# Kernel optimization log

Hardware: AMD Instinct MI355X
Metric: run time of the kernel (lower is better)

The kernel has to match this reference:

```python
import jax, jax.numpy as jnp
import numpy as np
import math

D_MODEL = 1024
NHEAD = 16
FACTOR = 5


def setup_inputs() -> dict:
    key = jax.random.key(0)
    kq, kk, kv = jax.random.split(key, 3)
    B, L = 4, 2048
    Q = jax.random.normal(kq, (B, L, D_MODEL), dtype=jnp.float32)
    K = jax.random.normal(kk, (B, L, D_MODEL), dtype=jnp.float32)
    V = jax.random.normal(kv, (B, L, D_MODEL), dtype=jnp.float32)
    return {"Q": Q, "K": K, "V": V}


def reference(Q, K, V):
    B, q_len, _ = Q.shape
    k_len = K.shape[1]
    head_dim = D_MODEL // NHEAD
    scale = 1.0 / math.sqrt(head_dim)

    # [B, H, L, Dh]
    Qh = Q.reshape(B, q_len, NHEAD, head_dim).transpose(0, 2, 1, 3)
    Kh = K.reshape(B, k_len, NHEAD, head_dim).transpose(0, 2, 1, 3)
    Vh = V.reshape(B, k_len, NHEAD, head_dim).transpose(0, 2, 1, 3)

    # Dense scores for KL-based query selection
    scores = jnp.einsum('bhqd,bhkd->bhqk', Qh, Kh) * scale
    logp = jax.nn.log_softmax(scores, axis=-1)
    probs = jnp.exp(logp)
    # KL(p || uniform) = sum p * (log p + log k_len)
    kl_div = jnp.sum(probs * (logp + jnp.log(jnp.float32(k_len))), axis=-1)  # [B,H,Q]

    top_u = min(int(FACTOR * math.log(q_len)), q_len)
    _, indices = jax.lax.top_k(kl_div, top_u)  # [B,H,U]

    # Gather selected queries
    Q_sparse = jnp.take_along_axis(Qh, indices[..., None], axis=2)  # [B,H,U,Dh]
    scores_sparse = jnp.einsum('bhud,bhkd->bhuk', Q_sparse, Kh) * scale
    attn_weights = jax.nn.softmax(scores_sparse, axis=-1)  # dropout p=0 (eval)
    output_sparse = jnp.einsum('bhuk,bhkd->bhud', attn_weights, Vh)

    # Scatter back into full-length output (non-selected queries are zero)
    b_idx = jnp.arange(B)[:, None, None]
    h_idx = jnp.arange(NHEAD)[None, :, None]
    output_full = jnp.zeros_like(Qh).at[b_idx, h_idx, indices].set(output_sparse)

    output = output_full.transpose(0, 2, 1, 3).reshape(B, q_len, D_MODEL)
    return output, attn_weights
```

## Files before the change

### kernel.cpp

```cpp
#include <hip/hip_runtime.h>
#include <math.h>

#define LQ 2048
#define DM 1024
#define NH 16
#define DH 64
#define UU 38
#define NBH 64
#define SCALE 0.125f

typedef _Float16 f16x8 __attribute__((ext_vector_type(8)));
typedef float f32x4 __attribute__((ext_vector_type(4)));
typedef float f32x2 __attribute__((ext_vector_type(2)));

#if __has_builtin(__builtin_amdgcn_exp2f)
#define EXP2F(x) __builtin_amdgcn_exp2f(x)
#else
#define EXP2F(x) exp2f(x)
#endif

#define GL2LDS16(gp, lp)                                           \
  __builtin_amdgcn_global_load_lds(                                \
      (const __attribute__((address_space(1))) void*)(gp),         \
      (__attribute__((address_space(3))) void*)(lp), 16, 0, 0)

#define F_OFF_SEL   4194304
#define F_OFF_L3    4204032
#define F_OFF_MASK  4213760
#define F_OFF_LPART 4344832
#define F_OFF_KSP   7146496
#define F_NEED      40700928ull

__global__ __launch_bounds__(256) void ksplit_kernel(const float* __restrict__ K,
                                                     _Float16* __restrict__ ksp,
                                                     float* __restrict__ outz) {
  int idx = blockIdx.x * 256 + threadIdx.x;
  int p = idx & 7;
  int k = (idx >> 3) & 63;
  int kc = (idx >> 9) & 31;
  int bh = idx >> 14;
  int b = bh >> 4, h = bh & 15;
  const float* src = K + ((size_t)(b * LQ + kc * 64 + k)) * DM + h * DH + (p ^ (k & 7)) * 8;
  float4 x0 = *(const float4*)src;
  float4 x1 = *(const float4*)(src + 4);
  f16x8 hi, lo;
#define KCV(i, xx) { float x_ = (xx); _Float16 hh = (_Float16)x_; hi[i] = hh; lo[i] = (_Float16)(x_ - (float)hh); }
  KCV(0, x0.x) KCV(1, x0.y) KCV(2, x0.z) KCV(3, x0.w)
  KCV(4, x1.x) KCV(5, x1.y) KCV(6, x1.z) KCV(7, x1.w)
#undef KCV
  _Float16* base = ksp + ((size_t)(bh * 32 + kc)) * 8192;
  *(f16x8*)(base + k * 64 + p * 8) = hi;
  *(f16x8*)(base + 4096 + k * 64 + p * 8) = lo;

  float4 z = {0.f, 0.f, 0.f, 0.f};
  *(float4*)(outz + (size_t)idx * 8) = z;
  *(float4*)(outz + (size_t)idx * 8 + 4) = z;
}

__global__ __launch_bounds__(256) void kl_mfma2(const float* __restrict__ Q,
                                                const _Float16* __restrict__ ksp,
                                                double* __restrict__ lt) {
  int bh = blockIdx.x & 63;
  int qc = (blockIdx.x >> 6) & 15;
  int sp = blockIdx.x >> 10;
  int b = bh >> 4, h = bh & 15;
  int t = threadIdx.x;
  int lane = t & 63, w = t >> 6;
  int quad = lane >> 4, l15 = lane & 15;

  __shared__ __align__(16) _Float16 kbuf[8192];

  f16x8 ahi[2][2], alo[2][2];
  {
    const float* qrow = Q + ((size_t)(b * LQ + qc * 128)) * DM + h * DH;
#pragma unroll
    for (int qt = 0; qt < 2; ++qt)
#pragma unroll
      for (int c = 0; c < 2; ++c) {
        const float* p = qrow + (size_t)(w * 32 + qt * 16 + l15) * DM + c * 32 + quad * 8;
        float4 x0 = *(const float4*)p;
        float4 x1 = *(const float4*)(p + 4);
        f16x8 hi, lo;
#define QCV(i, xx) { float x_ = (xx); _Float16 hh = (_Float16)x_; hi[i] = hh; lo[i] = (_Float16)(x_ - (float)hh); }
        QCV(0, x0.x) QCV(1, x0.y) QCV(2, x0.z) QCV(3, x0.w)
        QCV(4, x1.x) QCV(5, x1.y) QCV(6, x1.z) QCV(7, x1.w)
#undef QCV
        ahi[qt][c] = hi;
        alo[qt][c] = lo;
      }
  }

  int bsw0 = quad ^ (l15 & 7);
  int bsw1 = (quad + 4) ^ (l15 & 7);
  const float C1 = 0.18033688011112042f;

  double l64[2][4], t64[2][4];
#pragma unroll
  for (int qt = 0; qt < 2; ++qt)
#pragma unroll
    for (int r = 0; r < 4; ++r) { l64[qt][r] = 0.0; t64[qt][r] = 0.0; }

  const _Float16* khiA = kbuf;
  const _Float16* kloA = kbuf + 2048;
  const _Float16* khiB = kbuf + 4096;
  const _Float16* kloB = kbuf + 6144;

  const char* gp = (const char*)(ksp + ((size_t)(bh * 32 + sp * 16)) * 8192) + t * 16;
  char* ldsA = (char*)kbuf + w * 1024;
  char* ldsB = (char*)kbuf + 8192 + w * 1024;

#define KLSTEP(KHI, KLO)                                                        \
  _Pragma("unroll")                                                             \
  for (int kt = 0; kt < 2; ++kt) {                                              \
    int key = kt * 16 + l15;                                                    \
    f16x8 bhi0 = *(const f16x8*)((KHI) + key * 64 + bsw0 * 8);                  \
    f16x8 bhi1 = *(const f16x8*)((KHI) + key * 64 + bsw1 * 8);                  \
    f16x8 blo0 = *(const f16x8*)((KLO) + key * 64 + bsw0 * 8);                  \
    f16x8 blo1 = *(const f16x8*)((KLO) + key * 64 + bsw1 * 8);                  \
    _Pragma("unroll")                                                           \
    for (int qt = 0; qt < 2; ++qt) {                                            \
      f32x4 cacc = {0.f, 0.f, 0.f, 0.f};                                        \
      __builtin_amdgcn_s_setprio(1);                                            \
      cacc = __builtin_amdgcn_mfma_f32_16x16x32_f16(alo[qt][0], bhi0, cacc, 0, 0, 0); \
      cacc = __builtin_amdgcn_mfma_f32_16x16x32_f16(alo[qt][1], bhi1, cacc, 0, 0, 0); \
      cacc = __builtin_amdgcn_mfma_f32_16x16x32_f16(ahi[qt][0], blo0, cacc, 0, 0, 0); \
      cacc = __builtin_amdgcn_mfma_f32_16x16x32_f16(ahi[qt][1], blo1, cacc, 0, 0, 0); \
      cacc = __builtin_amdgcn_mfma_f32_16x16x32_f16(ahi[qt][0], bhi0, cacc, 0, 0, 0); \
      cacc = __builtin_amdgcn_mfma_f32_16x16x32_f16(ahi[qt][1], bhi1, cacc, 0, 0, 0); \
      __builtin_amdgcn_s_setprio(0);                                            \
      _Pragma("unroll")                                                         \
      for (int rp = 0; rp < 2; ++rp) {                                          \
        f32x2 rr = { cacc[2 * rp], cacc[2 * rp + 1] };                          \
        f32x2 sc = rr * C1;                                   \
        f32x2 e  = { EXP2F(sc[0]), EXP2F(sc[1]) };                              \
        l32[qt][rp] += e;                                     \
        t32[qt][rp] += rr * e;                                \
      }                                                                         \
    }                                                                           \
  }

  GL2LDS16(gp, ldsA);
  GL2LDS16(gp + 8192, ldsA + 4096);
  __syncthreads();

  for (int j = 0; j < 16; ++j) {
    GL2LDS16(gp + 4096, ldsB);
    GL2LDS16(gp + 12288, ldsB + 4096);

    f32x2 l32[2][2], t32[2][2];
#pragma unroll
    for (int qt = 0; qt < 2; ++qt)
#pragma unroll
      for (int rp = 0; rp < 2; ++rp) {
        l32[qt][rp] = (f32x2){0.f, 0.f};
        t32[qt][rp] = (f32x2){0.f, 0.f};
      }

    KLSTEP(khiA, kloA)
    __syncthreads();

    if (j < 15) {
      gp += 16384;
      GL2LDS16(gp, ldsA);
      GL2LDS16(gp + 8192, ldsA + 4096);
    }

    KLSTEP(khiB, kloB)

#pragma unroll
    for (int qt = 0; qt < 2; ++qt)
#pragma unroll
      for (int rp = 0; rp < 2; ++rp)
#pragma unroll
        for (int c = 0; c < 2; ++c) {
          l64[qt][rp * 2 + c] += (double)l32[qt][rp][c];
          t64[qt][rp * 2 + c] += (double)t32[qt][rp][c];
        }
    __syncthreads();
  }
#undef KLSTEP

#pragma unroll
  for (int qt = 0; qt < 2; ++qt)
#pragma unroll
    for (int r = 0; r < 4; ++r) {
      double lv = l64[qt][r], tv = t64[qt][r];
#pragma unroll
      for (int m = 1; m < 16; m <<= 1) {
        lv += __shfl_xor(lv, m);
        tv += __shfl_xor(tv, m);
      }
      if (l15 == 0) {
        int qg = qc * 128 + w * 32 + qt * 16 + quad * 4 + r;
        double* dst = lt + ((size_t)(sp * 64 + bh) * LQ + qg) * 2;
        dst[0] = lv;
        dst[1] = tv;
      }
    }
}

__global__ __launch_bounds__(64) void topk2(const double* __restrict__ lt,
                                            int* __restrict__ idxout,
                                            float* __restrict__ l3out) {
  int bh = blockIdx.x;
  int lane = threadIdx.x;
  __shared__ double vals[LQ];
  __shared__ float lsh[LQ];
  const double logL = 7.624618986159398;

  double v1 = -INFINITY, v2 = -INFINITY, v3 = -INFINITY;
  int i1 = LQ, i2 = LQ, i3 = LQ;

  for (int j = 0; j < 32; ++j) {
    int i = j * 64 + lane;
    const double* p0 = lt + ((size_t)bh * LQ + i) * 2;
    const double* p1 = lt + ((size_t)(64 + bh) * LQ + i) * 2;
    double l = p0[0] + p1[0];
    double tt = p0[1] + p1[1];
    double v = 0.125 * (tt / l) - log(l) + logL;
    vals[i] = v;
    lsh[i] = (float)l;
    if (v > v1)      { v3 = v2; i3 = i2; v2 = v1; i2 = i1; v1 = v; i1 = i; }
    else if (v > v2) { v3 = v2; i3 = i2; v2 = v;  i2 = i; }
    else if (v > v3) { v3 = v;  i3 = i; }
  }

  for (int u = 0; u < UU; ++u) {
    if (i1 == LQ) {
      v1 = v2 = v3 = -INFINITY;
      i1 = i2 = i3 = LQ;
      for (int j = 0; j < 32; ++j) {
        int i = j * 64 + lane;
        double v = vals[i];
        if (v > v1)      { v3 = v2; i3 = i2; v2 = v1; i2 = i1; v1 = v; i1 = i; }
        else if (v > v2) { v3 = v2; i3 = i2; v2 = v;  i2 = i; }
        else if (v > v3) { v3 = v;  i3 = i; }
      }
    }

    double gv = v1;
    int gi = i1;
#pragma unroll
    for (int m = 1; m < 64; m <<= 1) {
      double ov = __shfl_xor(gv, m);
      int oi = __shfl_xor(gi, m);
      if (ov > gv || (ov == gv && oi < gi)) { gv = ov; gi = oi; }
    }
    if (lane == 0) idxout[bh * UU + u] = gi;
    if ((gi & 63) == lane) {
      l3out[bh * UU + u] = lsh[gi];
      vals[gi] = -INFINITY;
      v1 = v2; i1 = i2;
      v2 = v3; i2 = i3;
      v3 = -INFINITY; i3 = LQ;
    }
  }
}

__global__ __launch_bounds__(256) void attn_w_pv(const float* __restrict__ Q,
                                                 const _Float16* __restrict__ ksp,
                                                 const int* __restrict__ sel,
                                                 const float* __restrict__ l3,
                                                 const float* __restrict__ V,
                                                 float* __restrict__ wout,
                                                 float* __restrict__ out) {
  int bh = blockIdx.x >> 4;
  int ks = blockIdx.x & 15;
  int b = bh >> 4, h = bh & 15;
  int t = threadIdx.x;
  int lane = t & 63, w = t >> 6;
  int quad = lane >> 4, l15 = lane & 15;

  __shared__ __align__(16) _Float16 kbuf[8192];
  __shared__ float els[48 * 132];
  __shared__ int sidx[UU];
  __shared__ float l3i[48];

  if (t < UU) sidx[t] = sel[bh * UU + t];
  if (t < 48) l3i[t] = (t < UU) ? 1.f / l3[bh * UU + t] : 0.f;
  __syncthreads();

  f16x8 ahi[3][2], alo[3][2];
#pragma unroll
  for (int qt = 0; qt < 3; ++qt) {
    int u = qt * 16 + l15;
    if (u > 37) u = 37;
    const float* qrow = Q + ((size_t)(b * LQ + sidx[u])) * DM + h * DH;
#pragma unroll
    for (int c = 0; c < 2; ++c) {
      const float* p = qrow + c * 32 + quad * 8;
      float4 x0 = *(const float4*)p;
      float4 x1 = *(const float4*)(p + 4);
      f16x8 hi, lo;
#define QCV(i, xx) { float x_ = (xx); _Float16 hh = (_Float16)x_; hi[i] = hh; lo[i] = (_Float16)(x_ - (float)hh); }
      QCV(0, x0.x) QCV(1, x0.y) QCV(2, x0.z) QCV(3, x0.w)
      QCV(4, x1.x) QCV(5, x1.y) QCV(6, x1.z) QCV(7, x1.w)
#undef QCV
      ahi[qt][c] = hi;
      alo[qt][c] = lo;
    }
  }

  int bsw0 = quad ^ (l15 & 7);
  int bsw1 = (quad + 4) ^ (l15 & 7);
  const float C1 = 0.18033688011112042f;
  const char* gch = (const char*)(ksp + ((size_t)(bh * 32 + ks * 2)) * 8192);
  _Float16* khi = kbuf;
  _Float16* klo = kbuf + 4096;

  for (int chunk = 0; chunk < 2; ++chunk) {
    __syncthreads();
    {
      const char* gs = gch + (size_t)chunk * 16384 + (size_t)t * 16;
      char* ls = (char*)kbuf + (size_t)(w * 64) * 16;
#pragma unroll
      for (int i = 0; i < 4; ++i)
        GL2LDS16(gs + i * 4096, ls + i * 4096);
    }
    __syncthreads();
    int key = w * 16 + l15;
    f16x8 bhi0 = *(const f16x8*)(khi + key * 64 + bsw0 * 8);
    f16x8 bhi1 = *(const f16x8*)(khi + key * 64 + bsw1 * 8);
    f16x8 blo0 = *(const f16x8*)(klo + key * 64 + bsw0 * 8);
    f16x8 blo1 = *(const f16x8*)(klo + key * 64 + bsw1 * 8);
#pragma unroll
    for (int qt = 0; qt < 3; ++qt) {
      f32x4 cacc = {0.f, 0.f, 0.f, 0.f};
      cacc = __builtin_amdgcn_mfma_f32_16x16x32_f16(alo[qt][0], bhi0, cacc, 0, 0, 0);
      cacc = __builtin_amdgcn_mfma_f32_16x16x32_f16(alo[qt][1], bhi1, cacc, 0, 0, 0);
      cacc = __builtin_amdgcn_mfma_f32_16x16x32_f16(ahi[qt][0], blo0, cacc, 0, 0, 0);
      cacc = __builtin_amdgcn_mfma_f32_16x16x32_f16(ahi[qt][1], blo1, cacc, 0, 0, 0);
      cacc = __builtin_amdgcn_mfma_f32_16x16x32_f16(ahi[qt][0], bhi0, cacc, 0, 0, 0);
      cacc = __builtin_amdgcn_mfma_f32_16x16x32_f16(ahi[qt][1], bhi1, cacc, 0, 0, 0);
#pragma unroll
      for (int r = 0; r < 4; ++r) {
        int row = qt * 16 + quad * 4 + r;
        els[row * 132 + chunk * 64 + w * 16 + l15] = EXP2F(cacc[r] * C1);
      }
    }
  }
  __syncthreads();

  for (int i = t; i < UU * 128; i += 256) {
    int u = i >> 7, k = i & 127;
    wout[((size_t)(bh * UU + u)) * LQ + ks * 128 + k] = els[u * 132 + k] * l3i[u];
  }

  int d = t & 63, ug = t >> 6;
  const float* vbase = V + ((size_t)(b * LQ + ks * 128)) * DM + h * DH + d;
  float o[10];
#pragma unroll
  for (int p = 0; p < 10; ++p) o[p] = 0.f;

  for (int j4 = 0; j4 < 128; j4 += 4) {
    float v0 = vbase[(size_t)(j4 + 0) * DM];
    float v1 = vbase[(size_t)(j4 + 1) * DM];
    float v2 = vbase[(size_t)(j4 + 2) * DM];
    float v3 = vbase[(size_t)(j4 + 3) * DM];
#pragma unroll
    for (int p = 0; p < 10; ++p) {
      float4 pw = *(const float4*)(els + (ug + 4 * p) * 132 + j4);
      o[p] = fmaf(pw.x, v0, o[p]);
      o[p] = fmaf(pw.y, v1, o[p]);
      o[p] = fmaf(pw.z, v2, o[p]);
      o[p] = fmaf(pw.w, v3, o[p]);
    }
  }

#pragma unroll
  for (int p = 0; p < 10; ++p) {
    int u = ug + 4 * p;
    if (u < UU) {
      float* dst = out + ((size_t)(b * LQ + sidx[u])) * DM + h * DH + d;
      atomicAdd(dst, o[p] * l3i[u]);
    }
  }
}

extern "C" void kernel_launch(void* const* d_in, const int* in_sizes, int n_in,
                              void* d_out, int out_size, void* d_ws, size_t ws_size,
                              hipStream_t stream) {
  (void)in_sizes; (void)n_in;
  if (ws_size < F_NEED) return;
  const float* Q = (const float*)d_in[0];
  const float* K = (const float*)d_in[1];
  const float* V = (const float*)d_in[2];
  float* out = (float*)d_out;
  float* wout = out + (size_t)4 * LQ * DM;
  char* ws = (char*)d_ws;

  double* lt = (double*)ws;
  int* sel = (int*)(ws + F_OFF_SEL);
  float* l3 = (float*)(ws + F_OFF_L3);
  _Float16* ksp = (_Float16*)(ws + F_OFF_KSP);

  ksplit_kernel<<<4096, 256, 0, stream>>>(K, ksp, out);
  kl_mfma2<<<2048, 256, 0, stream>>>(Q, ksp, lt);
  topk2<<<NBH, 64, 0, stream>>>(lt, sel, l3);
  attn_w_pv<<<NBH * 16, 256, 0, stream>>>(Q, ksp, sel, l3, V, wout, out);
}
```

Baseline: 341.2 us.

## Triple-buffer K tiles in KL kernel with one barrier per step

Replaces the double-buffered LDS pipeline in the KL scoring kernel with a three-slot ring buffer. Each half-tile step now waits on an explicit vmcnt and a single barrier, keeping two global-to-LDS loads in flight. The previous scheme used two __syncthreads per iteration. The aim is to hide load latency better and cut synchronisation stalls. The cost is 50% more LDS per block, which may lower occupancy, and the manual waitcnt accounting is fragile.

```diff
diff --git a/kernel.cpp b/kernel.cpp
--- a/kernel.cpp
+++ b/kernel.cpp
@@ -68,7 +68,7 @@
   int lane = t & 63, w = t >> 6;
   int quad = lane >> 4, l15 = lane & 15;
 
-  __shared__ __align__(16) _Float16 kbuf[8192];
+  __shared__ __align__(16) _Float16 kbuf[12288];
 
   f16x8 ahi[2][2], alo[2][2];
   {
@@ -100,23 +100,33 @@
 #pragma unroll
     for (int r = 0; r < 4; ++r) { l64[qt][r] = 0.0; t64[qt][r] = 0.0; }
 
-  const _Float16* khiA = kbuf;
-  const _Float16* kloA = kbuf + 2048;
-  const _Float16* khiB = kbuf + 4096;
-  const _Float16* kloB = kbuf + 6144;
-
-  const char* gp = (const char*)(ksp + ((size_t)(bh * 32 + sp * 16)) * 8192) + t * 16;
-  char* ldsA = (char*)kbuf + w * 1024;
-  char* ldsB = (char*)kbuf + 8192 + w * 1024;
-
-#define KLSTEP(KHI, KLO)                                                        \
+  f32x2 l32[2][2], t32[2][2];
+#pragma unroll
+  for (int qt = 0; qt < 2; ++qt)
+#pragma unroll
+    for (int rp = 0; rp < 2; ++rp) {
+      l32[qt][rp] = (f32x2){0.f, 0.f};
+      t32[qt][rp] = (f32x2){0.f, 0.f};
+    }
+
+  const char* gch8 = (const char*)(ksp + ((size_t)(bh * 32 + sp * 16)) * 8192) + t * 16;
+  char* lbb = (char*)kbuf + w * 1024;
+
+#define STAGE(m_, n_)                                                           \
+  { const char* s_ = gch8 + (((m_) >> 1) * 16384) + (((m_) & 1) * 4096);        \
+    GL2LDS16(s_, lbb + (n_) * 8192);                                            \
+    GL2LDS16(s_ + 8192, lbb + (n_) * 8192 + 4096); }
+
+#define KLSTEP(N_)                                                              \
   _Pragma("unroll")                                                             \
   for (int kt = 0; kt < 2; ++kt) {                                              \
     int key = kt * 16 + l15;                                                    \
-    f16x8 bhi0 = *(const f16x8*)((KHI) + key * 64 + bsw0 * 8);                  \
-    f16x8 bhi1 = *(const f16x8*)((KHI) + key * 64 + bsw1 * 8);                  \
-    f16x8 blo0 = *(const f16x8*)((KLO) + key * 64 + bsw0 * 8);                  \
-    f16x8 blo1 = *(const f16x8*)((KLO) + key * 64 + bsw1 * 8);                  \
+    const _Float16* KHI = kbuf + (N_) * 4096;                                   \
+    const _Float16* KLO = KHI + 2048;                                           \
+    f16x8 bhi0 = *(const f16x8*)(KHI + key * 64 + bsw0 * 8);                    \
+    f16x8 bhi1 = *(const f16x8*)(KHI + key * 64 + bsw1 * 8);                    \
+    f16x8 blo0 = *(const f16x8*)(KLO + key * 64 + bsw0 * 8);                    \
+    f16x8 blo1 = *(const f16x8*)(KLO + key * 64 + bsw1 * 8);                    \
     _Pragma("unroll")                                                           \
     for (int qt = 0; qt < 2; ++qt) {                                            \
       f32x4 cacc = {0.f, 0.f, 0.f, 0.f};                                        \
@@ -131,54 +141,51 @@
       _Pragma("unroll")                                                         \
       for (int rp = 0; rp < 2; ++rp) {                                          \
         f32x2 rr = { cacc[2 * rp], cacc[2 * rp + 1] };                          \
-        f32x2 sc = rr * C1;                                   \
+        f32x2 sc = rr * C1;                                                     \
         f32x2 e  = { EXP2F(sc[0]), EXP2F(sc[1]) };                              \
-        l32[qt][rp] += e;                                     \
-        t32[qt][rp] += rr * e;                                \
+        l32[qt][rp] += e;                                                       \
+        t32[qt][rp] += rr * e;                                                  \
       }                                                                         \
     }                                                                           \
   }
 
-  GL2LDS16(gp, ldsA);
-  GL2LDS16(gp + 8192, ldsA + 4096);
-  __syncthreads();
-
-  for (int j = 0; j < 16; ++j) {
-    GL2LDS16(gp + 4096, ldsB);
-    GL2LDS16(gp + 12288, ldsB + 4096);
-
-    f32x2 l32[2][2], t32[2][2];
-#pragma unroll
-    for (int qt = 0; qt < 2; ++qt)
-#pragma unroll
-      for (int rp = 0; rp < 2; ++rp) {
-        l32[qt][rp] = (f32x2){0.f, 0.f};
-        t32[qt][rp] = (f32x2){0.f, 0.f};
-      }
-
-    KLSTEP(khiA, kloA)
-    __syncthreads();
-
-    if (j < 15) {
-      gp += 16384;
-      GL2LDS16(gp, ldsA);
-      GL2LDS16(gp + 8192, ldsA + 4096);
-    }
-
-    KLSTEP(khiB, kloB)
-
-#pragma unroll
-    for (int qt = 0; qt < 2; ++qt)
-#pragma unroll
-      for (int rp = 0; rp < 2; ++rp)
-#pragma unroll
-        for (int c = 0; c < 2; ++c) {
-          l64[qt][rp * 2 + c] += (double)l32[qt][rp][c];
-          t64[qt][rp * 2 + c] += (double)t32[qt][rp][c];
-        }
-    __syncthreads();
-  }
+#define FOLD()                                                                  \
+  { _Pragma("unroll")                                                           \
+    for (int qt = 0; qt < 2; ++qt)                                              \
+      _Pragma("unroll")                                                         \
+      for (int rp = 0; rp < 2; ++rp)                                            \
+        _Pragma("unroll")                                                       \
+        for (int c = 0; c < 2; ++c) {                                           \
+          l64[qt][rp * 2 + c] += (double)l32[qt][rp][c];                        \
+          t64[qt][rp * 2 + c] += (double)t32[qt][rp][c];                        \
+          l32[qt][rp][c] = 0.f;                                                 \
+          t32[qt][rp][c] = 0.f;                                                 \
+        } }
+
+#define SUB2(i_, n_, vm_)                                                       \
+  asm volatile("s_waitcnt vmcnt(" vm_ ")" ::: "memory");                        \
+  __builtin_amdgcn_sched_barrier(0);                                            \
+  __builtin_amdgcn_s_barrier();
+
+  STAGE(0, 0)
+  STAGE(1, 1)
+
+  for (int k5 = 0; k5 < 5; ++k5) {
+    int i0 = 6 * k5;
+    SUB2(i0 + 0, 0, "2") STAGE(i0 + 2, 2) KLSTEP(0)
+    SUB2(i0 + 1, 1, "2") STAGE(i0 + 3, 0) KLSTEP(1) FOLD()
+    SUB2(i0 + 2, 2, "2") STAGE(i0 + 4, 1) KLSTEP(2)
+    SUB2(i0 + 3, 0, "2") STAGE(i0 + 5, 2) KLSTEP(0) FOLD()
+    SUB2(i0 + 4, 1, "2") STAGE(i0 + 6, 0) KLSTEP(1)
+    SUB2(i0 + 5, 2, "2") STAGE(i0 + 7, 1) KLSTEP(2) FOLD()
+  }
+  SUB2(30, 0, "2") KLSTEP(0)
+  SUB2(31, 1, "0") KLSTEP(1) FOLD()
+
+#undef SUB2
+#undef STAGE
 #undef KLSTEP
+#undef FOLD
 
 #pragma unroll
   for (int qt = 0; qt < 2; ++qt)
```

Measured after the change: 340.9 us. About the same (-0.1%).
